# Kernel tuning notes

Measured on AMD Instinct MI355X. Metric: run time of the kernel, lower is better.

The kernel has to match this reference:

```python
import jax, jax.numpy as jnp
import numpy as np

N_ATOMS = 100000
K_NBR = 64
N_STRUCT = 32
HID = 128


def _energy(x, W1, w2, mask, batch_idx):
    # x: [N, K, 3] neighbor displacement vectors; surrogate per-edge energy MLP
    h = jnp.tanh(jnp.einsum('nkc,cd->nkd', x, W1))          # [N, K, HID]
    e = jnp.einsum('nkd,d->nk', h, w2)                       # [N, K]
    e = jnp.where(mask, 0.0, e)                              # zero padded neighbors
    per_atom = e.sum(axis=1)                                 # [N]
    return jax.ops.segment_sum(per_atom, batch_idx, num_segments=N_STRUCT)  # [S]


def setup_inputs() -> dict:
    key = jax.random.key(0)
    k = jax.random.split(key, 7)
    x = jax.random.normal(k[0], (N_ATOMS, K_NBR, 3), dtype=jnp.float32)
    neighbors_index = jax.random.randint(k[1], (K_NBR, N_ATOMS), 0, N_ATOMS)
    neighbors_pos = jax.random.randint(k[2], (N_ATOMS, K_NBR), 0, K_NBR)
    mask = jax.random.randint(k[3], (N_ATOMS, K_NBR), 0, 2).astype(bool)
    batch_idx = jax.random.randint(k[4], (N_ATOMS,), 0, N_STRUCT)
    W1 = jax.random.normal(k[5], (3, HID), dtype=jnp.float32) * 0.1
    w2 = jax.random.normal(k[6], (HID,), dtype=jnp.float32) * 0.1
    return {"x": x, "neighbors_index": neighbors_index, "neighbors_pos": neighbors_pos,
            "mask": mask, "batch_idx": batch_idx, "W1": W1, "w2": w2}


def reference(x, neighbors_index, neighbors_pos, mask, batch_idx, W1, w2):
    # predictions: per-structure scalar energies
    preds = _energy(x, W1, w2, mask, batch_idx)
    # grads = d(sum of predictions)/dx  (grad_outputs = ones_like(predictions))
    grads = jax.grad(lambda xx: _energy(xx, W1, w2, mask, batch_idx).sum())(x)  # [N, K, 3]
    nbr = neighbors_index.T                                   # [N, K]
    # irregular gather of reverse-edge gradients (uses UNMASKED grads, as in torch code)
    grads_messaged = grads[nbr, neighbors_pos]                # [N, K, 3]
    m = mask[..., None]
    first = jnp.where(m, 0.0, grads).sum(axis=1)              # [N, 3]
    second = jnp.where(m, 0.0, grads_messaged).sum(axis=1)    # [N, 3]
    forces = first - second
    return preds, forces
```

## Files before the change

### kernel.cpp

```cpp
#include <hip/hip_runtime.h>
#include <hip/hip_bf16.h>

#define N_ATOMS 100000
#define K_NBR   64
#define N_STRUCT 32
#define HID     128
#define N_EDGE  (N_ATOMS * K_NBR)
#define ATOMS_PB 32
#define EDGES_PB (ATOMS_PB * K_NBR)
#define NBLK_EL (N_ATOMS / ATOMS_PB)
#define NBLK_A  ((N_ATOMS + 63) / 64)

typedef unsigned int uint;

#if __has_builtin(__builtin_amdgcn_exp2f)
#define EXP2(v) __builtin_amdgcn_exp2f(v)
#else
#define EXP2(v) __expf((v) * 0.69314718056f)
#endif

__device__ __forceinline__ uint bf_rne(float f) {
    uint u = __float_as_uint(f);
    return (u + 0x7fffu + ((u >> 16) & 1u)) >> 16;
}
__device__ __forceinline__ float ubf_lo(uint u) { return __uint_as_float(u << 16); }
__device__ __forceinline__ float ubf_hi(uint u) { return __uint_as_float(u & 0xffff0000u); }

__global__ void prep_kernel(const float* __restrict__ W1, const float* __restrict__ w2,
                            float4* __restrict__ pw4, float4* __restrict__ gw4,
                            float* __restrict__ sumw2)
{
    const float L2E2 = 2.885390082f;
    int d = threadIdx.x;
    float w0 = W1[d], w1 = W1[HID + d], wc = W1[2 * HID + d], wv = w2[d];
    pw4[d] = make_float4(L2E2 * w0, L2E2 * w1, L2E2 * wc, wv);
    gw4[d] = make_float4(4.f * wv * w0, 4.f * wv * w1, 4.f * wv * wc, 0.f);
    float v = wv;
    for (int off = 32; off; off >>= 1) v += __shfl_down(v, off, 64);
    __shared__ float sw_[2];
    if ((threadIdx.x & 63) == 0) sw_[threadIdx.x >> 6] = v;
    __syncthreads();
    if (threadIdx.x == 0) sumw2[0] = sw_[0] + sw_[1];
}

__global__ __launch_bounds__(256) void edge_local(
    const float* __restrict__ x, const int* __restrict__ mask,
    const int* __restrict__ batch,
    const float4* __restrict__ pw4, const float4* __restrict__ gw4,
    const float* __restrict__ sumw2p,
    uint2* __restrict__ gr8, float* __restrict__ part)
{
    __shared__ unsigned short list[EDGES_PB];
    __shared__ int   lcnt;
    __shared__ float sp[N_STRUCT];
    __shared__ int   sbatch[ATOMS_PB];

    const int tid = threadIdx.x, lane = tid & 63;
    const int ebase = blockIdx.x * EDGES_PB;

    if (tid == 0) lcnt = 0;
    if (tid < N_STRUCT) sp[tid] = 0.f;
    if (tid < ATOMS_PB) sbatch[tid] = batch[blockIdx.x * ATOMS_PB + tid];
    __syncthreads();

    #pragma unroll
    for (int p = 0; p < EDGES_PB / 256; ++p) {
        int le = p * 256 + tid;
        int m = mask[ebase + le];
        unsigned long long bal = __ballot(m == 0);
        int wcnt = __popcll(bal);
        int pre  = __popcll(bal & ((1ull << lane) - 1ull));
        int wbase;
        if (lane == 0) wbase = atomicAdd(&lcnt, wcnt);
        wbase = __shfl(wbase, 0, 64);
        if (m == 0) list[wbase + pre] = (unsigned short)le;
        else        gr8[ebase + le] = make_uint2(0u, 0u);
    }
    __syncthreads();

    const int L = lcnt;
    const float sumw2 = sumw2p[0];

    for (int i = tid; i < L; i += 256) {
        int le  = list[i];
        int eid = ebase + le;
        const float* xp = x + (size_t)eid * 3;
        float x0 = xp[0], x1 = xp[1], x2 = xp[2];
        float rsum = 0.f, g0 = 0.f, g1 = 0.f, g2 = 0.f;
        for (int d = 0; d < HID; d += 4) {
            float4 wa = pw4[d], wb = pw4[d + 1], wc = pw4[d + 2], wd = pw4[d + 3];
            float4 Ga = gw4[d], Gb = gw4[d + 1], Gc = gw4[d + 2], Gd = gw4[d + 3];
            float ea = EXP2(fmaf(x0, wa.x, fmaf(x1, wa.y, x2 * wa.z)));
            float eb = EXP2(fmaf(x0, wb.x, fmaf(x1, wb.y, x2 * wb.z)));
            float ec = EXP2(fmaf(x0, wc.x, fmaf(x1, wc.y, x2 * wc.z)));
            float ed = EXP2(fmaf(x0, wd.x, fmaf(x1, wd.y, x2 * wd.z)));
            float aa = ea + 1.f, ab = eb + 1.f, ac = ec + 1.f, ad = ed + 1.f;
            float pab = aa * ab, pcd = ac * ad;
            float q   = __builtin_amdgcn_rcpf(pab * pcd);
            float qab = q * pcd, qcd = q * pab;
            float ra = qab * ab, rb = qab * aa, rc = qcd * ad, rd = qcd * ac;
            rsum = fmaf(wa.w, ra, rsum);
            rsum = fmaf(wb.w, rb, rsum);
            rsum = fmaf(wc.w, rc, rsum);
            rsum = fmaf(wd.w, rd, rsum);
            float sa = fmaf(-ra, ra, ra);
            float sb = fmaf(-rb, rb, rb);
            float sc = fmaf(-rc, rc, rc);
            float sd = fmaf(-rd, rd, rd);
            g0 = fmaf(sa, Ga.x, g0); g1 = fmaf(sa, Ga.y, g1); g2 = fmaf(sa, Ga.z, g2);
            g0 = fmaf(sb, Gb.x, g0); g1 = fmaf(sb, Gb.y, g1); g2 = fmaf(sb, Gb.z, g2);
            g0 = fmaf(sc, Gc.x, g0); g1 = fmaf(sc, Gc.y, g1); g2 = fmaf(sc, Gc.z, g2);
            g0 = fmaf(sd, Gd.x, g0); g1 = fmaf(sd, Gd.y, g1); g2 = fmaf(sd, Gd.z, g2);
        }
        float e = fmaf(-2.f, rsum, sumw2);
        uint lo = bf_rne(g0) | (bf_rne(g1) << 16);
        uint hi = bf_rne(g2);
        gr8[eid] = make_uint2(lo, hi);
        atomicAdd(&sp[sbatch[le >> 6]], e);
    }
    __syncthreads();
    if (tid < N_STRUCT) part[(size_t)tid * NBLK_EL + blockIdx.x] = sp[tid];
}

__global__ __launch_bounds__(256) void atom_fused(
    const uint2* __restrict__ gr8, const int* __restrict__ nidx,
    const int* __restrict__ pos, const int* __restrict__ mask,
    const float* __restrict__ part, float* __restrict__ out)
{
    __shared__ int tile[64][65];
    __shared__ float sv[4];
    const int tid = threadIdx.x, lane = tid & 63, w = tid >> 6;
    const int n0 = blockIdx.x * 64;

    #pragma unroll
    for (int i = 0; i < 16; ++i) {
        int k = i * 4 + w, n = n0 + lane;
        tile[k][lane] = (n < N_ATOMS) ? nidx[k * N_ATOMS + n] : 0;
    }
    __syncthreads();

    #pragma unroll 2
    for (int j = 0; j < 8; ++j) {
        int nlA = w * 16 + 2 * j;
        int nA  = n0 + nlA;
        int nB  = nA + 1;
        bool vA = (nA < N_ATOMS), vB = (nB < N_ATOMS);

        float fA0 = 0.f, fA1 = 0.f, fA2 = 0.f, fB0 = 0.f, fB1 = 0.f, fB2 = 0.f;
        if (vA) {
            int eiA = nA * 64 + lane;
            int mA = mask[eiA], psA = pos[eiA];
            int nbA = tile[lane][nlA];
            uint2 aA = gr8[eiA];
            uint2 bA = make_uint2(0u, 0u);
            if (!mA) bA = gr8[(size_t)nbA * 64 + psA];
            fA0 = ubf_lo(aA.x) - ubf_lo(bA.x);
            fA1 = ubf_hi(aA.x) - ubf_hi(bA.x);
            fA2 = ubf_lo(aA.y) - ubf_lo(bA.y);
        }
        if (vB) {
            int eiB = nB * 64 + lane;
            int mB = mask[eiB], psB = pos[eiB];
            int nbB = tile[lane][nlA + 1];
            uint2 aB = gr8[eiB];
            uint2 bB = make_uint2(0u, 0u);
            if (!mB) bB = gr8[(size_t)nbB * 64 + psB];
            fB0 = ubf_lo(aB.x) - ubf_lo(bB.x);
            fB1 = ubf_hi(aB.x) - ubf_hi(bB.x);
            fB2 = ubf_lo(aB.y) - ubf_lo(bB.y);
        }

        for (int off = 32; off; off >>= 1) {
            fA0 += __shfl_down(fA0, off, 64);
            fA1 += __shfl_down(fA1, off, 64);
            fA2 += __shfl_down(fA2, off, 64);
            fB0 += __shfl_down(fB0, off, 64);
            fB1 += __shfl_down(fB1, off, 64);
            fB2 += __shfl_down(fB2, off, 64);
        }
        if (lane == 0 && vA) {
            float* fo = out + N_STRUCT + (size_t)nA * 3;
            fo[0] = fA0; fo[1] = fA1; fo[2] = fA2;
            if (vB) { fo[3] = fB0; fo[4] = fB1; fo[5] = fB2; }
        }
    }

    if (blockIdx.x < N_STRUCT) {
        int s = blockIdx.x;
        float v = 0.f;
        for (int i = tid; i < NBLK_EL; i += 256) v += part[(size_t)s * NBLK_EL + i];
        for (int off = 32; off; off >>= 1) v += __shfl_down(v, off, 64);
        if (lane == 0) sv[w] = v;
        __syncthreads();
        if (tid == 0) out[s] = sv[0] + sv[1] + sv[2] + sv[3];
    }
}

extern "C" void kernel_launch(void* const* d_in, const int* in_sizes, int n_in,
                              void* d_out, int out_size, void* d_ws, size_t ws_size,
                              hipStream_t stream)
{
    const float* x    = (const float*)d_in[0];
    const int*   nidx = (const int*)d_in[1];
    const int*   npos = (const int*)d_in[2];
    const int*   mask = (const int*)d_in[3];
    const int*   bidx = (const int*)d_in[4];
    const float* W1   = (const float*)d_in[5];
    const float* w2   = (const float*)d_in[6];
    float* out = (float*)d_out;

    char* ws = (char*)d_ws;
    uint2* gr8  = (uint2*)ws;
    float* part = (float*)(ws + (size_t)N_EDGE * 8);
    char*  tail = ws + (size_t)N_EDGE * 8
                     + (size_t)N_STRUCT * NBLK_EL * sizeof(float);
    float4* pw4   = (float4*)tail;
    float4* gw4   = (float4*)(tail + HID * 16);
    float*  sumw2 = (float*)(tail + 2 * HID * 16);

    hipLaunchKernelGGL(prep_kernel, dim3(1), dim3(128), 0, stream,
                       W1, w2, pw4, gw4, sumw2);
    hipLaunchKernelGGL(edge_local, dim3(NBLK_EL), dim3(256), 0, stream,
                       x, mask, bidx, pw4, gw4, sumw2, gr8, part);
    hipLaunchKernelGGL(atom_fused, dim3(NBLK_A), dim3(256), 0, stream,
                       gr8, nidx, npos, mask, part, out);
}
```

Baseline: 383.7 us.

## Precompute gather indices and first-term force sums inside edge kernel

Moves the neighbor-index transpose, mask and position reads into the edge kernel, which now writes a flat gather index per edge and accumulates each atom's local gradient sum in shared memory. The second kernel becomes a gather-only pass that reads one index per edge plus the precomputed first-term sums, so it no longer reloads mask, pos, nidx and the local gradients. The edge kernel now covers 64 atoms per block and writes an extra index array plus four shared atomics per edge, which adds workspace traffic and contention in exchange for a lighter gather pass.

```diff
diff --git a/kernel.cpp b/kernel.cpp
--- a/kernel.cpp
+++ b/kernel.cpp
@@ -6,10 +6,10 @@
 #define N_STRUCT 32
 #define HID     128
 #define N_EDGE  (N_ATOMS * K_NBR)
-#define ATOMS_PB 32
+#define ATOMS_PB 64
 #define EDGES_PB (ATOMS_PB * K_NBR)
-#define NBLK_EL (N_ATOMS / ATOMS_PB)
-#define NBLK_A  ((N_ATOMS + 63) / 64)
+#define NBLK_EL ((N_ATOMS + ATOMS_PB - 1) / ATOMS_PB)
+#define NBLK_G  (N_ATOMS / 8)
 
 typedef unsigned int uint;
 
@@ -45,36 +45,60 @@
 
 __global__ __launch_bounds__(256) void edge_local(
     const float* __restrict__ x, const int* __restrict__ mask,
+    const int* __restrict__ nidx, const int* __restrict__ pos,
     const int* __restrict__ batch,
     const float4* __restrict__ pw4, const float4* __restrict__ gw4,
     const float* __restrict__ sumw2p,
-    uint2* __restrict__ gr8, float* __restrict__ part)
-{
+    uint2* __restrict__ gr8, int* __restrict__ gidx,
+    float4* __restrict__ first4, float* __restrict__ part)
+{
+    __shared__ int tile[64][65];
     __shared__ unsigned short list[EDGES_PB];
-    __shared__ int   lcnt;
+    __shared__ float sfirst[ATOMS_PB][4];
     __shared__ float sp[N_STRUCT];
     __shared__ int   sbatch[ATOMS_PB];
-
-    const int tid = threadIdx.x, lane = tid & 63;
-    const int ebase = blockIdx.x * EDGES_PB;
+    __shared__ int   lcnt;
+
+    const int tid = threadIdx.x, lane = tid & 63, w = tid >> 6;
+    const int n0 = blockIdx.x * ATOMS_PB;
+    const int ebase = n0 * K_NBR;
 
     if (tid == 0) lcnt = 0;
     if (tid < N_STRUCT) sp[tid] = 0.f;
-    if (tid < ATOMS_PB) sbatch[tid] = batch[blockIdx.x * ATOMS_PB + tid];
+    if (tid < ATOMS_PB) {
+        int n = n0 + tid;
+        sbatch[tid] = (n < N_ATOMS) ? batch[n] : 0;
+        sfirst[tid][0] = 0.f; sfirst[tid][1] = 0.f; sfirst[tid][2] = 0.f;
+    }
+    #pragma unroll
+    for (int i = 0; i < 16; ++i) {
+        int k = i * 4 + w, n = n0 + lane;
+        tile[k][lane] = (n < N_ATOMS) ? nidx[k * N_ATOMS + n] : 0;
+    }
     __syncthreads();
 
     #pragma unroll
     for (int p = 0; p < EDGES_PB / 256; ++p) {
         int le = p * 256 + tid;
-        int m = mask[ebase + le];
-        unsigned long long bal = __ballot(m == 0);
+        int nl = le >> 6, k = le & 63;
+        bool valid = (n0 + nl) < N_ATOMS;
+        int ei = ebase + le;
+        int un = 0;
+        if (valid) {
+            int m = mask[ei];
+            un = (m == 0);
+            int g = -1;
+            if (un) g = tile[k][nl] * 64 + pos[ei];
+            else    gr8[ei] = make_uint2(0u, 0u);
+            gidx[ei] = g;
+        }
+        unsigned long long bal = __ballot(un);
         int wcnt = __popcll(bal);
         int pre  = __popcll(bal & ((1ull << lane) - 1ull));
         int wbase;
         if (lane == 0) wbase = atomicAdd(&lcnt, wcnt);
         wbase = __shfl(wbase, 0, 64);
-        if (m == 0) list[wbase + pre] = (unsigned short)le;
-        else        gr8[ebase + le] = make_uint2(0u, 0u);
+        if (un) list[wbase + pre] = (unsigned short)le;
     }
     __syncthreads();
 
@@ -116,73 +140,52 @@
         uint lo = bf_rne(g0) | (bf_rne(g1) << 16);
         uint hi = bf_rne(g2);
         gr8[eid] = make_uint2(lo, hi);
-        atomicAdd(&sp[sbatch[le >> 6]], e);
-    }
-    __syncthreads();
+        int a = le >> 6;
+        atomicAdd(&sp[sbatch[a]], e);
+        atomicAdd(&sfirst[a][0], g0);
+        atomicAdd(&sfirst[a][1], g1);
+        atomicAdd(&sfirst[a][2], g2);
+    }
+    __syncthreads();
+
+    if (tid < ATOMS_PB && (n0 + tid) < N_ATOMS)
+        first4[n0 + tid] = make_float4(sfirst[tid][0], sfirst[tid][1],
+                                       sfirst[tid][2], 0.f);
     if (tid < N_STRUCT) part[(size_t)tid * NBLK_EL + blockIdx.x] = sp[tid];
 }
 
-__global__ __launch_bounds__(256) void atom_fused(
-    const uint2* __restrict__ gr8, const int* __restrict__ nidx,
-    const int* __restrict__ pos, const int* __restrict__ mask,
-    const float* __restrict__ part, float* __restrict__ out)
-{
-    __shared__ int tile[64][65];
-    __shared__ float sv[4];
+__global__ __launch_bounds__(256) void atom_gather(
+    const uint2* __restrict__ gr8, const int* __restrict__ gidx,
+    const float4* __restrict__ first4, const float* __restrict__ part,
+    float* __restrict__ out)
+{
     const int tid = threadIdx.x, lane = tid & 63, w = tid >> 6;
-    const int n0 = blockIdx.x * 64;
-
-    #pragma unroll
-    for (int i = 0; i < 16; ++i) {
-        int k = i * 4 + w, n = n0 + lane;
-        tile[k][lane] = (n < N_ATOMS) ? nidx[k * N_ATOMS + n] : 0;
-    }
-    __syncthreads();
-
-    #pragma unroll 2
-    for (int j = 0; j < 8; ++j) {
-        int nlA = w * 16 + 2 * j;
-        int nA  = n0 + nlA;
-        int nB  = nA + 1;
-        bool vA = (nA < N_ATOMS), vB = (nB < N_ATOMS);
-
-        float fA0 = 0.f, fA1 = 0.f, fA2 = 0.f, fB0 = 0.f, fB1 = 0.f, fB2 = 0.f;
-        if (vA) {
-            int eiA = nA * 64 + lane;
-            int mA = mask[eiA], psA = pos[eiA];
-            int nbA = tile[lane][nlA];
-            uint2 aA = gr8[eiA];
-            uint2 bA = make_uint2(0u, 0u);
-            if (!mA) bA = gr8[(size_t)nbA * 64 + psA];
-            fA0 = ubf_lo(aA.x) - ubf_lo(bA.x);
-            fA1 = ubf_hi(aA.x) - ubf_hi(bA.x);
-            fA2 = ubf_lo(aA.y) - ubf_lo(bA.y);
-        }
-        if (vB) {
-            int eiB = nB * 64 + lane;
-            int mB = mask[eiB], psB = pos[eiB];
-            int nbB = tile[lane][nlA + 1];
-            uint2 aB = gr8[eiB];
-            uint2 bB = make_uint2(0u, 0u);
-            if (!mB) bB = gr8[(size_t)nbB * 64 + psB];
-            fB0 = ubf_lo(aB.x) - ubf_lo(bB.x);
-            fB1 = ubf_hi(aB.x) - ubf_hi(bB.x);
-            fB2 = ubf_lo(aB.y) - ubf_lo(bB.y);
-        }
-
-        for (int off = 32; off; off >>= 1) {
-            fA0 += __shfl_down(fA0, off, 64);
-            fA1 += __shfl_down(fA1, off, 64);
-            fA2 += __shfl_down(fA2, off, 64);
-            fB0 += __shfl_down(fB0, off, 64);
-            fB1 += __shfl_down(fB1, off, 64);
-            fB2 += __shfl_down(fB2, off, 64);
-        }
-        if (lane == 0 && vA) {
-            float* fo = out + N_STRUCT + (size_t)nA * 3;
-            fo[0] = fA0; fo[1] = fA1; fo[2] = fA2;
-            if (vB) { fo[3] = fB0; fo[4] = fB1; fo[5] = fB2; }
-        }
+    const int nA = blockIdx.x * 8 + w * 2;
+    const int nB = nA + 1;
+
+    int gA = gidx[nA * 64 + lane];
+    int gB = gidx[nB * 64 + lane];
+    uint2 bA = make_uint2(0u, 0u), bB = make_uint2(0u, 0u);
+    if (gA >= 0) bA = gr8[gA];
+    if (gB >= 0) bB = gr8[gB];
+
+    float sA0 = ubf_lo(bA.x), sA1 = ubf_hi(bA.x), sA2 = ubf_lo(bA.y);
+    float sB0 = ubf_lo(bB.x), sB1 = ubf_hi(bB.x), sB2 = ubf_lo(bB.y);
+
+    for (int off = 32; off; off >>= 1) {
+        sA0 += __shfl_down(sA0, off, 64);
+        sA1 += __shfl_down(sA1, off, 64);
+        sA2 += __shfl_down(sA2, off, 64);
+        sB0 += __shfl_down(sB0, off, 64);
+        sB1 += __shfl_down(sB1, off, 64);
+        sB2 += __shfl_down(sB2, off, 64);
+    }
+    if (lane == 0) {
+        float4 fA = first4[nA];
+        float4 fB = first4[nB];
+        float* fo = out + N_STRUCT + (size_t)nA * 3;
+        fo[0] = fA.x - sA0; fo[1] = fA.y - sA1; fo[2] = fA.z - sA2;
+        fo[3] = fB.x - sB0; fo[4] = fB.y - sB1; fo[5] = fB.z - sB2;
     }
 
     if (blockIdx.x < N_STRUCT) {
@@ -190,6 +193,7 @@
         float v = 0.f;
         for (int i = tid; i < NBLK_EL; i += 256) v += part[(size_t)s * NBLK_EL + i];
         for (int off = 32; off; off >>= 1) v += __shfl_down(v, off, 64);
+        __shared__ float sv[4];
         if (lane == 0) sv[w] = v;
         __syncthreads();
         if (tid == 0) out[s] = sv[0] + sv[1] + sv[2] + sv[3];
@@ -210,10 +214,13 @@
     float* out = (float*)d_out;
 
     char* ws = (char*)d_ws;
-    uint2* gr8  = (uint2*)ws;
-    float* part = (float*)(ws + (size_t)N_EDGE * 8);
-    char*  tail = ws + (size_t)N_EDGE * 8
-                     + (size_t)N_STRUCT * NBLK_EL * sizeof(float);
+    uint2*  gr8    = (uint2*)ws;
+    int*    gidx   = (int*)(ws + (size_t)N_EDGE * 8);
+    float4* first4 = (float4*)(ws + (size_t)N_EDGE * 12);
+    float*  part   = (float*)(ws + (size_t)N_EDGE * 12
+                                 + (size_t)N_ATOMS * 16);
+    char*   tail   = ws + (size_t)N_EDGE * 12 + (size_t)N_ATOMS * 16
+                        + (size_t)N_STRUCT * NBLK_EL * 4;
     float4* pw4   = (float4*)tail;
     float4* gw4   = (float4*)(tail + HID * 16);
     float*  sumw2 = (float*)(tail + 2 * HID * 16);
@@ -221,7 +228,8 @@
     hipLaunchKernelGGL(prep_kernel, dim3(1), dim3(128), 0, stream,
                        W1, w2, pw4, gw4, sumw2);
     hipLaunchKernelGGL(edge_local, dim3(NBLK_EL), dim3(256), 0, stream,
-                       x, mask, bidx, pw4, gw4, sumw2, gr8, part);
-    hipLaunchKernelGGL(atom_fused, dim3(NBLK_A), dim3(256), 0, stream,
-                       gr8, nidx, npos, mask, part, out);
-}
+                       x, mask, nidx, npos, bidx, pw4, gw4, sumw2,
+                       gr8, gidx, first4, part);
+    hipLaunchKernelGGL(atom_gather, dim3(NBLK_G), dim3(256), 0, stream,
+                       gr8, gidx, first4, part, out);
+}
```

Result: slower. 423.4 us (+10.4%).
